# Optimization experiments

Hardware: AMD Instinct MI355X
Metric: run time of the kernel (lower is better)

The kernel has to match this reference:

```python
import jax, jax.numpy as jnp
import numpy as np

N, DM, F, G, FG = 4096, 512, 128, 8, 16
DH, DE, ES = 128, 256, 4
E = G * ES
GROUP_TOP_K, EXPERT_TOP_K = 2, 2
TEMP = 1.0
LN_EPS = 1e-5


def _ln(x, g, b):
    m = jnp.mean(x, axis=-1, keepdims=True)
    v = jnp.mean((x - m) ** 2, axis=-1, keepdims=True)
    return (x - m) * jax.lax.rsqrt(v + LN_EPS) * g + b


def _topk_softmax(logits, k):
    # faithful to torch _topk_softmax: softmax over top-k values, zeros elsewhere
    vals, idx = jax.lax.top_k(logits, k)
    w = jax.nn.softmax(vals, axis=-1)
    oh = jax.nn.one_hot(idx, logits.shape[-1], dtype=logits.dtype)  # [..., k, E]
    return jnp.einsum('...ke,...k->...e', oh, w)


def setup_inputs() -> dict:
    key = jax.random.key(0)
    ks = iter(jax.random.split(key, 32))
    n = lambda shape, s=0.02: jax.random.normal(next(ks), shape, dtype=jnp.float32) * s
    d = {
        'hidden': jax.random.normal(next(ks), (N, DM), dtype=jnp.float32),
        'feat': jax.random.normal(next(ks), (N, F), dtype=jnp.float32),
        # pre_ln
        'pre_ln_g': jnp.ones((DM,), jnp.float32), 'pre_ln_b': jnp.zeros((DM,), jnp.float32),
        # router_hidden_encoder: LN(DM) -> Lin(DM,DH) -> GELU -> Lin(DH,DH)
        'rh_ln_g': jnp.ones((DM,), jnp.float32), 'rh_ln_b': jnp.zeros((DM,), jnp.float32),
        'rh_w1': n((DM, DH)), 'rh_b1': jnp.zeros((DH,), jnp.float32),
        'rh_w2': n((DH, DH)), 'rh_b2': jnp.zeros((DH,), jnp.float32),
        # stage_feature_encoder: LN(F) -> Lin(F,DH) -> GELU -> Lin(DH,DH)
        'sf_ln_g': jnp.ones((F,), jnp.float32), 'sf_ln_b': jnp.zeros((F,), jnp.float32),
        'sf_w1': n((F, DH)), 'sf_b1': jnp.zeros((DH,), jnp.float32),
        'sf_w2': n((DH, DH)), 'sf_b2': jnp.zeros((DH,), jnp.float32),
        # group_feature_encoders (stacked over G): LN(FG) -> Lin(FG,DH) -> GELU -> Lin(DH,DH)
        'gf_ln_g': jnp.ones((G, FG), jnp.float32), 'gf_ln_b': jnp.zeros((G, FG), jnp.float32),
        'gf_w1': n((G, FG, DH)), 'gf_b1': jnp.zeros((G, DH), jnp.float32),
        'gf_w2': n((G, DH, DH)), 'gf_b2': jnp.zeros((G, DH), jnp.float32),
        # per_group_scorer (ScalarRouter): Lin(4DH,DH) -> GELU -> Lin(DH,1)
        'pgs_w1': n((4 * DH, DH)), 'pgs_b1': jnp.zeros((DH,), jnp.float32),
        'pgs_w2': n((DH,)), 'pgs_b2': jnp.zeros((), jnp.float32),
        # intra_routers (stacked over G): Lin(4DH,DH) -> GELU -> Lin(DH,ES)
        'ir_w1': n((G, 4 * DH, DH)), 'ir_b1': jnp.zeros((G, DH), jnp.float32),
        'ir_w2': n((G, DH, ES)), 'ir_b2': jnp.zeros((G, ES), jnp.float32),
        # experts (stacked over E = G*ES, group-major): Lin(DM,DE) -> GELU -> Lin(DE,DM)
        'ex_w1': n((E, DM, DE)), 'ex_b1': jnp.zeros((E, DE), jnp.float32),
        'ex_w2': n((E, DE, DM)), 'ex_b2': jnp.zeros((E, DM), jnp.float32),
    }
    return d


def reference(hidden, feat, pre_ln_g, pre_ln_b, rh_ln_g, rh_ln_b, rh_w1, rh_b1, rh_w2, rh_b2,
              sf_ln_g, sf_ln_b, sf_w1, sf_b1, sf_w2, sf_b2,
              gf_ln_g, gf_ln_b, gf_w1, gf_b1, gf_w2, gf_b2,
              pgs_w1, pgs_b1, pgs_w2, pgs_b2,
              ir_w1, ir_b1, ir_w2, ir_b2,
              ex_w1, ex_b1, ex_w2, ex_b2):
    # expert input (pre-LN hidden)
    h_norm = _ln(hidden, pre_ln_g, pre_ln_b)                         # [N, DM]

    # factorized router encoders
    h_enc = jax.nn.gelu(_ln(hidden, rh_ln_g, rh_ln_b) @ rh_w1 + rh_b1) @ rh_w2 + rh_b2   # [N, DH]
    s_enc = jax.nn.gelu(_ln(feat, sf_ln_g, sf_ln_b) @ sf_w1 + sf_b1) @ sf_w2 + sf_b2     # [N, DH]
    gfeat = feat.reshape(N, G, FG)                                    # disjoint contiguous group features
    g_h = jax.nn.gelu(jnp.einsum('ngf,gfh->ngh', _ln(gfeat, gf_ln_g, gf_ln_b), gf_w1) + gf_b1)
    g_enc = jnp.einsum('ngh,ghk->ngk', g_h, gf_w2) + gf_b2            # [N, G, DH]

    hB = jnp.broadcast_to(h_enc[:, None, :], (N, G, DH))
    sB = jnp.broadcast_to(s_enc[:, None, :], (N, G, DH))
    router_in = jnp.concatenate([hB, sB, g_enc, hB * g_enc], axis=-1)  # [N, G, 4DH]

    # per-group scalar scores -> group logits -> top-k scatter softmax
    pg_h = jax.nn.gelu(jnp.einsum('ngi,ih->ngh', router_in, pgs_w1) + pgs_b1)
    group_logits = (jnp.einsum('ngh,h->ng', pg_h, pgs_w2) + pgs_b2) / max(TEMP, 1e-6)    # [N, G]
    group_w = _topk_softmax(group_logits, GROUP_TOP_K)                 # [N, G]

    # intra-group expert routers -> top-k scatter softmax over expert_scale
    ir_h = jax.nn.gelu(jnp.einsum('ngi,gih->ngh', router_in, ir_w1) + ir_b1)
    intra_logits = jnp.einsum('ngh,ghe->nge', ir_h, ir_w2) + ir_b2     # [N, G, ES]
    intra_w = _topk_softmax(intra_logits, EXPERT_TOP_K)                # [N, G, ES]

    comb_w = (group_w[:, :, None] * intra_w).reshape(N, E)             # group-major expert order

    # per-expert GELU MLPs on pre-LN hidden (dense compute, sparse weights)
    eh = jax.nn.gelu(jnp.einsum('nd,edh->neh', h_norm, ex_w1) + ex_b1) # [N, E, DE]
    eo = jnp.einsum('neh,ehd->ned', eh, ex_w2) + ex_b2                 # [N, E, DM]
    out = jnp.einsum('ne,ned->nd', comb_w, eo)                         # [N, DM]
    return out
```

## Files before the change

kernel.cpp:

```cpp
#include <hip/hip_runtime.h>
#include <hip/hip_bf16.h>
#include <math.h>

#define N_TOK 4096
#define DM 512
#define FDIM 128
#define G 8
#define FG 16
#define DH 128
#define DE 256
#define ES 4
#define E_EXP 32
#define LN_EPS 1e-5f
#define BT 32

typedef __attribute__((ext_vector_type(8))) short bf16x8;
typedef __attribute__((ext_vector_type(4))) float f32x4;

#define MFMA16(a, b, c) __builtin_amdgcn_mfma_f32_16x16x32_bf16((a), (b), (c), 0, 0, 0)

__device__ __forceinline__ float gelu_t(float x) {
    const float c = 0.7978845608028654f;
    float x3 = x * x * x;
    return 0.5f * x * (1.0f + tanhf(c * (x + 0.044715f * x3)));
}

__device__ __forceinline__ short f2bf(float f) {
    __hip_bfloat16 h = __float2bfloat16(f);
    return *reinterpret_cast<short*>(&h);
}
__device__ __forceinline__ float bf2f(short s) {
    __hip_bfloat16 h = *reinterpret_cast<__hip_bfloat16*>(&s);
    return __bfloat162float(h);
}
__device__ __forceinline__ void split3(float x, short& h, short& m, short& l) {
    h = f2bf(x);
    float r = x - bf2f(h);
    m = f2bf(r);
    float r2 = r - bf2f(m);
    l = f2bf(r2);
}

struct ConvJob { const float* src; short* dh; short* dm; short* dl;
                 int KB, NB, Kreal, plain, blk0; };
struct ConvJobs { ConvJob j[10]; };

__global__ void k_pre(ConvJobs J, int nconv,
                      const float* __restrict__ hidden,
                      const float* __restrict__ pg, const float* __restrict__ pb,
                      const float* __restrict__ rg, const float* __restrict__ rb,
                      __hip_bfloat16* __restrict__ h_normb, float* __restrict__ hL) {
    int b = blockIdx.x;
    if (b >= nconv) {
        int n = b - nconv;
        int j = threadIdx.x;
        const float* x = hidden + (size_t)n * DM;
        float v0 = x[j], v1 = x[j + 256];
        float s = v0 + v1, q = v0 * v0 + v1 * v1;
#pragma unroll
        for (int o = 32; o; o >>= 1) { s += __shfl_down(s, o); q += __shfl_down(q, o); }
        __shared__ float red[8];
        int w = j >> 6;
        if ((j & 63) == 0) { red[w] = s; red[4 + w] = q; }
        __syncthreads();
        float sum = red[0] + red[1] + red[2] + red[3];
        float sq  = red[4] + red[5] + red[6] + red[7];
        float m = sum * (1.0f / DM);
        float var = sq * (1.0f / DM) - m * m;
        float rs = rsqrtf(var + LN_EPS);
        float t0 = (v0 - m) * rs, t1 = (v1 - m) * rs;
        size_t base = (size_t)n * DM;
        h_normb[base + j]       = __float2bfloat16(t0 * pg[j]       + pb[j]);
        h_normb[base + j + 256] = __float2bfloat16(t1 * pg[j + 256] + pb[j + 256]);
        hL[base + j]           = t0 * rg[j]       + rb[j];
        hL[base + j + 256]     = t1 * rg[j + 256] + rb[j + 256];
        return;
    }
    int ji = 0;
#pragma unroll
    for (int i = 1; i < 10; i++) if (b >= J.j[i].blk0) ji = i;
    const ConvJob jb = J.j[ji];
    int rel = b - jb.blk0;
    int mat = rel / jb.KB, kb = rel % jb.KB;
    int ncols = jb.NB * 16;
    const float* s = jb.src + (size_t)mat * jb.Kreal * ncols;
    size_t dbase = ((size_t)mat * jb.KB + kb) * jb.NB * 512;
    for (int p = threadIdx.x; p < jb.NB * 64; p += 256) {
        int nb = p >> 6, lane = p & 63;
        int row0 = kb * 32 + ((lane >> 4) << 3);
        int col = nb * 16 + (lane & 15);
        if (jb.plain) {
            union { short sh[8]; uint4 v; } t;
#pragma unroll
            for (int j = 0; j < 8; j++) {
                float x = (row0 + j < jb.Kreal) ? s[(size_t)(row0 + j) * ncols + col] : 0.f;
                t.sh[j] = f2bf(x);
            }
            *(uint4*)&jb.dh[dbase + (size_t)p * 8] = t.v;
        } else {
            union { short sh[8]; uint4 v; } hi, mi, lo;
#pragma unroll
            for (int j = 0; j < 8; j++) {
                float x = (row0 + j < jb.Kreal) ? s[(size_t)(row0 + j) * ncols + col] : 0.f;
                split3(x, hi.sh[j], mi.sh[j], lo.sh[j]);
            }
            *(uint4*)&jb.dh[dbase + (size_t)p * 8] = hi.v;
            *(uint4*)&jb.dm[dbase + (size_t)p * 8] = mi.v;
            *(uint4*)&jb.dl[dbase + (size_t)p * 8] = lo.v;
        }
    }
}

template <int KB_TOT, bool DO_LN>
__device__ __forceinline__ void enc2_body(
        int bx, char* smem,
        const float* __restrict__ X,
        const float* __restrict__ lng, const float* __restrict__ lnb,
        const short* __restrict__ W1h, const short* __restrict__ W1m, const short* __restrict__ W1l,
        const float* __restrict__ B1,
        const short* __restrict__ W2h, const short* __restrict__ W2m, const short* __restrict__ W2l,
        const float* __restrict__ B2,
        float* __restrict__ Y) {
    constexpr int K = KB_TOT * 32;
    const int n0 = bx * 32;
    const int tid = threadIdx.x;
    const int wave = tid >> 6, lane = tid & 63;
    const int quad = lane >> 4, lm = lane & 15;
    const int mt = wave & 1;
    const int ngb = (wave >> 1) * 4;

    short (*Ah)[132] = (short(*)[132])smem;
    short (*Am)[132] = (short(*)[132])(smem + 32 * 132 * 2);
    short (*Al)[132] = (short(*)[132])(smem + 2 * 32 * 132 * 2);

    f32x4 acc[4];
#pragma unroll
    for (int i = 0; i < 4; i++) acc[i] = (f32x4)(0.f);

    if (DO_LN) {
        for (int idx = tid; idx < 1024; idx += 256) {
            int row = idx >> 5, c4 = (idx & 31) * 4;
            float4 v = *(const float4*)&X[(size_t)(n0 + row) * K + c4];
            float s = v.x + v.y + v.z + v.w;
            float q = v.x * v.x + v.y * v.y + v.z * v.z + v.w * v.w;
#pragma unroll
            for (int o = 16; o; o >>= 1) { s += __shfl_xor(s, o); q += __shfl_xor(q, o); }
            float mean = s * (1.0f / 128.0f);
            float var = q * (1.0f / 128.0f) - mean * mean;
            float rs = rsqrtf(var + LN_EPS);
            float xv[4] = {(v.x - mean) * rs * lng[c4 + 0] + lnb[c4 + 0],
                           (v.y - mean) * rs * lng[c4 + 1] + lnb[c4 + 1],
                           (v.z - mean) * rs * lng[c4 + 2] + lnb[c4 + 2],
                           (v.w - mean) * rs * lng[c4 + 3] + lnb[c4 + 3]};
#pragma unroll
            for (int j = 0; j < 4; j++) {
                short h, m, l; split3(xv[j], h, m, l);
                Ah[row][c4 + j] = h; Am[row][c4 + j] = m; Al[row][c4 + j] = l;
            }
        }
        __syncthreads();
#pragma unroll
        for (int kb = 0; kb < KB_TOT; kb++) {
            bf16x8 ah = *(const bf16x8*)&Ah[mt * 16 + lm][kb * 32 + quad * 8];
            bf16x8 am = *(const bf16x8*)&Am[mt * 16 + lm][kb * 32 + quad * 8];
            bf16x8 al = *(const bf16x8*)&Al[mt * 16 + lm][kb * 32 + quad * 8];
#pragma unroll
            for (int nt = 0; nt < 4; nt++) {
                size_t bi = (((size_t)kb * 8 + ngb + nt) * 64 + lane) * 8;
                bf16x8 bh = *(const bf16x8*)&W1h[bi];
                bf16x8 bm = *(const bf16x8*)&W1m[bi];
                bf16x8 bl = *(const bf16x8*)&W1l[bi];
                acc[nt] = MFMA16(al, bh, acc[nt]);
                acc[nt] = MFMA16(am, bm, acc[nt]);
                acc[nt] = MFMA16(ah, bl, acc[nt]);
                acc[nt] = MFMA16(am, bh, acc[nt]);
                acc[nt] = MFMA16(ah, bm, acc[nt]);
                acc[nt] = MFMA16(ah, bh, acc[nt]);
            }
        }
    } else {
        for (int kb = 0; kb < KB_TOT; kb++) {
            const float* xs = X + (size_t)(n0 + mt * 16 + lm) * K + kb * 32 + quad * 8;
            float4 x0 = *(const float4*)xs, x1 = *(const float4*)(xs + 4);
            float xv[8] = {x0.x, x0.y, x0.z, x0.w, x1.x, x1.y, x1.z, x1.w};
            bf16x8 ah, am, al;
#pragma unroll
            for (int j = 0; j < 8; j++) {
                short h, m, l; split3(xv[j], h, m, l);
                ah[j] = h; am[j] = m; al[j] = l;
            }
#pragma unroll
            for (int nt = 0; nt < 4; nt++) {
                size_t bi = (((size_t)kb * 8 + ngb + nt) * 64 + lane) * 8;
                bf16x8 bh = *(const bf16x8*)&W1h[bi];
                bf16x8 bm = *(const bf16x8*)&W1m[bi];
                bf16x8 bl = *(const bf16x8*)&W1l[bi];
                acc[nt] = MFMA16(al, bh, acc[nt]);
                acc[nt] = MFMA16(am, bm, acc[nt]);
                acc[nt] = MFMA16(ah, bl, acc[nt]);
                acc[nt] = MFMA16(am, bh, acc[nt]);
                acc[nt] = MFMA16(ah, bm, acc[nt]);
                acc[nt] = MFMA16(ah, bh, acc[nt]);
            }
        }
    }
    __syncthreads();
#pragma unroll
    for (int nt = 0; nt < 4; nt++) {
        int col = (ngb + nt) * 16 + lm;
        float b1 = B1[col];
#pragma unroll
        for (int r = 0; r < 4; r++) {
            int row = mt * 16 + quad * 4 + r;
            short h, m, l; split3(gelu_t(acc[nt][r] + b1), h, m, l);
            Ah[row][col] = h; Am[row][col] = m; Al[row][col] = l;
        }
    }
    __syncthreads();
    f32x4 acc2[4];
#pragma unroll
    for (int i = 0; i < 4; i++) acc2[i] = (f32x4)(0.f);
#pragma unroll
    for (int kb = 0; kb < 4; kb++) {
        bf16x8 ah = *(const bf16x8*)&Ah[mt * 16 + lm][kb * 32 + quad * 8];
        bf16x8 am = *(const bf16x8*)&Am[mt * 16 + lm][kb * 32 + quad * 8];
        bf16x8 al = *(const bf16x8*)&Al[mt * 16 + lm][kb * 32 + quad * 8];
#pragma unroll
        for (int nt = 0; nt < 4; nt++) {
            size_t bi = (((size_t)kb * 8 + ngb + nt) * 64 + lane) * 8;
            bf16x8 bh = *(const bf16x8*)&W2h[bi];
            bf16x8 bm = *(const bf16x8*)&W2m[bi];
            bf16x8 bl = *(const bf16x8*)&W2l[bi];
            acc2[nt] = MFMA16(al, bh, acc2[nt]);
            acc2[nt] = MFMA16(am, bm, acc2[nt]);
            acc2[nt] = MFMA16(ah, bl, acc2[nt]);
            acc2[nt] = MFMA16(am, bh, acc2[nt]);
            acc2[nt] = MFMA16(ah, bm, acc2[nt]);
            acc2[nt] = MFMA16(ah, bh, acc2[nt]);
        }
    }
#pragma unroll
    for (int nt = 0; nt < 4; nt++) {
        int col = (ngb + nt) * 16 + lm;
        float b2 = B2[col];
#pragma unroll
        for (int r = 0; r < 4; r++) {
            int row = mt * 16 + quad * 4 + r;
            Y[(size_t)(n0 + row) * DH + col] = acc2[nt][r] + b2;
        }
    }
}

__device__ __forceinline__ void genc_one(
        int bx, int g, char* smem,
        const float* __restrict__ feat,
        const float* __restrict__ gln_g, const float* __restrict__ gln_b,
        const short* __restrict__ W1h, const short* __restrict__ W1m, const short* __restrict__ W1l,
        const float* __restrict__ gb1,
        const short* __restrict__ W2h, const short* __restrict__ W2m, const short* __restrict__ W2l,
        const float* __restrict__ gb2,
        float* __restrict__ g_enc) {
    const int tid = threadIdx.x;
    const int wave = tid >> 6, lane = tid & 63;
    const int quad = lane >> 4, lm = lane & 15;
    const int mt = wave & 1;
    const int ngb = (wave >> 1) * 4;
    const int n0 = bx * 32;

    short (*Ah)[132] = (short(*)[132])smem;
    short (*Am)[132] = (short(*)[132])(smem + 8448);
    short (*Al)[132] = (short(*)[132])(smem + 2 * 8448);

    {
        int t = tid >> 3, sub = tid & 7;
        const float* fr = feat + (size_t)(n0 + t) * FDIM + g * FG;
        float xv[FG];
        float mean = 0.f;
#pragma unroll
        for (int i = 0; i < FG; i++) { xv[i] = fr[i]; mean += xv[i]; }
        mean *= (1.0f / FG);
        float var = 0.f;
#pragma unroll
        for (int i = 0; i < FG; i++) { float d = xv[i] - mean; var += d * d; }
        var *= (1.0f / FG);
        float rs = rsqrtf(var + LN_EPS);
#pragma unroll
        for (int j = 0; j < 2; j++) {
            int i = sub * 2 + j;
            float xn = (xv[i] - mean) * rs * gln_g[g * FG + i] + gln_b[g * FG + i];
            short h, m, l; split3(xn, h, m, l);
            Ah[t][i] = h; Am[t][i] = m; Al[t][i] = l;
            Ah[t][16 + i] = 0; Am[t][16 + i] = 0; Al[t][16 + i] = 0;
        }
    }
    __syncthreads();
    f32x4 acc[4];
#pragma unroll
    for (int i = 0; i < 4; i++) acc[i] = (f32x4)(0.f);
    {
        bf16x8 ah = *(const bf16x8*)&Ah[mt * 16 + lm][quad * 8];
        bf16x8 am = *(const bf16x8*)&Am[mt * 16 + lm][quad * 8];
        bf16x8 al = *(const bf16x8*)&Al[mt * 16 + lm][quad * 8];
#pragma unroll
        for (int nt = 0; nt < 4; nt++) {
            size_t bi = (((size_t)g * 8 + ngb + nt) * 64 + lane) * 8;
            bf16x8 bh = *(const bf16x8*)&W1h[bi];
            bf16x8 bm = *(const bf16x8*)&W1m[bi];
            bf16x8 bl = *(const bf16x8*)&W1l[bi];
            acc[nt] = MFMA16(al, bh, acc[nt]);
            acc[nt] = MFMA16(am, bm, acc[nt]);
            acc[nt] = MFMA16(ah, bl, acc[nt]);
            acc[nt] = MFMA16(am, bh, acc[nt]);
            acc[nt] = MFMA16(ah, bm, acc[nt]);
            acc[nt] = MFMA16(ah, bh, acc[nt]);
        }
    }
    __syncthreads();
#pragma unroll
    for (int nt = 0; nt < 4; nt++) {
        int col = (ngb + nt) * 16 + lm;
        float b1 = gb1[g * DH + col];
#pragma unroll
        for (int r = 0; r < 4; r++) {
            int row = mt * 16 + quad * 4 + r;
            short h, m, l; split3(gelu_t(acc[nt][r] + b1), h, m, l);
            Ah[row][col] = h; Am[row][col] = m; Al[row][col] = l;
        }
    }
    __syncthreads();
    f32x4 acc2[4];
#pragma unroll
    for (int i = 0; i < 4; i++) acc2[i] = (f32x4)(0.f);
#pragma unroll
    for (int kb = 0; kb < 4; kb++) {
        bf16x8 a2h = *(const bf16x8*)&Ah[mt * 16 + lm][kb * 32 + quad * 8];
        bf16x8 a2m = *(const bf16x8*)&Am[mt * 16 + lm][kb * 32 + quad * 8];
        bf16x8 a2l = *(const bf16x8*)&Al[mt * 16 + lm][kb * 32 + quad * 8];
#pragma unroll
        for (int nt = 0; nt < 4; nt++) {
            size_t bi = ((((size_t)g * 4 + kb) * 8 + ngb + nt) * 64 + lane) * 8;
            bf16x8 bh = *(const bf16x8*)&W2h[bi];
            bf16x8 bm = *(const bf16x8*)&W2m[bi];
            bf16x8 bl = *(const bf16x8*)&W2l[bi];
            acc2[nt] = MFMA16(a2l, bh, acc2[nt]);
            acc2[nt] = MFMA16(a2m, bm, acc2[nt]);
            acc2[nt] = MFMA16(a2h, bl, acc2[nt]);
            acc2[nt] = MFMA16(a2m, bh, acc2[nt]);
            acc2[nt] = MFMA16(a2h, bm, acc2[nt]);
            acc2[nt] = MFMA16(a2h, bh, acc2[nt]);
        }
    }
#pragma unroll
    for (int nt = 0; nt < 4; nt++) {
        int col = (ngb + nt) * 16 + lm;
        float b2 = gb2[g * DH + col];
#pragma unroll
        for (int r = 0; r < 4; r++) {
            int row = mt * 16 + quad * 4 + r;
            g_enc[((size_t)(n0 + row) * G + g) * DH + col] = acc2[nt][r] + b2;
        }
    }
}

__global__ __launch_bounds__(256) void k_enc_all(
        const float* __restrict__ hL, const float* __restrict__ feat,
        const float* __restrict__ sf_g, const float* __restrict__ sf_b,
        const float* __restrict__ gln_g, const float* __restrict__ gln_b,
        const short* Brh1H, const short* Brh1M, const short* Brh1L, const float* rh_b1,
        const short* Brh2H, const short* Brh2M, const short* Brh2L, const float* rh_b2,
        const short* Bsf1H, const short* Bsf1M, const short* Bsf1L, const float* sf_b1,
        const short* Bsf2H, const short* Bsf2M, const short* Bsf2L, const float* sf_b2,
        const short* Bgf1H, const short* Bgf1M, const short* Bgf1L, const float* gf_b1,
        const short* Bgf2H, const short* Bgf2M, const short* Bgf2L, const float* gf_b2,
        float* __restrict__ h_enc, float* __restrict__ s_enc, float* __restrict__ g_enc) {
    __shared__ __align__(16) char smem[3 * 8448];
    int bid = blockIdx.x;
    if (bid < 128)
        enc2_body<16, false>(bid, smem, hL, nullptr, nullptr,
                             Brh1H, Brh1M, Brh1L, rh_b1, Brh2H, Brh2M, Brh2L, rh_b2, h_enc);
    else if (bid < 256)
        enc2_body<4, true>(bid - 128, smem, feat, sf_g, sf_b,
                           Bsf1H, Bsf1M, Bsf1L, sf_b1, Bsf2H, Bsf2M, Bsf2L, sf_b2, s_enc);
    else {
        int idx = bid - 256;
        genc_one(idx >> 3, idx & 7, smem, feat, gln_g, gln_b,
                 Bgf1H, Bgf1M, Bgf1L, gf_b1, Bgf2H, Bgf2M, Bgf2L, gf_b2, g_enc);
    }
}

__device__ __forceinline__ void stage16v(float4 a, float4 b, float4 c, float4 d,
                                         char* smem, int wo0, int wo1) {
    float v0[8] = {a.x, a.y, a.z, a.w, b.x, b.y, b.z, b.w};
    float v1[8] = {c.x, c.y, c.z, c.w, d.x, d.y, d.z, d.w};
    bf16x8 h0, m0, l0, h1, m1, l1;
#pragma unroll
    for (int j = 0; j < 8; j++) { short hh, mm, ll; split3(v0[j], hh, mm, ll); h0[j]=hh; m0[j]=mm; l0[j]=ll; }
#pragma unroll
    for (int j = 0; j < 8; j++) { short hh, mm, ll; split3(v1[j], hh, mm, ll); h1[j]=hh; m1[j]=mm; l1[j]=ll; }
    *(bf16x8*)(smem + wo0) = h0;           *(bf16x8*)(smem + wo1) = h1;
    *(bf16x8*)(smem + 16384 + wo0) = m0;   *(bf16x8*)(smem + 16384 + wo1) = m1;
    *(bf16x8*)(smem + 32768 + wo0) = l0;   *(bf16x8*)(smem + 32768 + wo1) = l1;
}

__global__ __launch_bounds__(512) void k_router_mfma(
        const float* __restrict__ h_enc, const float* __restrict__ s_enc,
        const float* __restrict__ g_enc,
        const short* __restrict__ BpgH, const short* __restrict__ BpgM, const short* __restrict__ BpgL,
        const short* __restrict__ BirH, const short* __restrict__ BirM, const short* __restrict__ BirL,
        const float* __restrict__ pb1, const float* __restrict__ pw2, const float* __restrict__ pb2,
        const float* __restrict__ ib1, const float* __restrict__ iw2, const float* __restrict__ ib2,
        float* __restrict__ glog, float* __restrict__ ilog) {
    const int g = blockIdx.x & 7;
    const int bx = blockIdx.x >> 3;
    const int n0 = bx * 64;
    const int tid = threadIdx.x;
    const int wave = tid >> 6, lane = tid & 63;
    const int quad = lane >> 4, lm = lane & 15;
    const bool is_pg = wave < 4;
    const int nbase = (wave & 3) * 2;
    const short* Bh = is_pg ? BpgH : (BirH + (size_t)g * 65536);
    const short* Bm = is_pg ? BpgM : (BirM + (size_t)g * 65536);
    const short* Bl = is_pg ? BpgL : (BirL + (size_t)g * 65536);

    __shared__ __align__(16) char smem[49152];

    const int sr = tid >> 3, scb = tid & 7;
    const float* hrow = h_enc + (size_t)(n0 + sr) * DH + scb * 16;
    const float* srow = s_enc + (size_t)(n0 + sr) * DH + scb * 16;
    const float* grow = g_enc + ((size_t)(n0 + sr) * G + g) * DH + scb * 16;
    const int skbl = scb >> 1, st16 = sr >> 4, slm = sr & 15, sq0 = (scb & 1) * 2;
    const int wo0 = skbl * 4096 + st16 * 1024 + (sq0 * 16 + slm) * 16;
    const int wo1 = wo0 + 256;

    f32x4 acc[4][2];
#pragma unroll
    for (int mt = 0; mt < 4; mt++)
#pragma unroll
        for (int nt = 0; nt < 2; nt++) acc[mt][nt] = (f32x4)(0.f);

    float4 A0, A1, A2, A3;

#define LOAD4(P) { const float4* p4_ = (const float4*)(P); \
                   A0 = p4_[0]; A1 = p4_[1]; A2 = p4_[2]; A3 = p4_[3]; }
#define COMPUTE_CHUNK(CH) { _Pragma("unroll") \
    for (int kbl = 0; kbl < 4; kbl++) { \
        const int kb = (CH) * 4 + kbl; \
        bf16x8 Ahf[4], Amf[4], Alf[4]; \
        _Pragma("unroll") \
        for (int mt = 0; mt < 4; mt++) { \
            size_t loff = (size_t)kbl * 4096 + mt * 1024 + (size_t)lane * 16; \
            Ahf[mt] = *(const bf16x8*)(smem + loff); \
            Amf[mt] = *(const bf16x8*)(smem + 16384 + loff); \
            Alf[mt] = *(const bf16x8*)(smem + 32768 + loff); \
        } \
        _Pragma("unroll") \
        for (int nt = 0; nt < 2; nt++) { \
            size_t bi = (((size_t)kb * 8 + nbase + nt) * 64 + lane) * 8; \
            bf16x8 bh = *(const bf16x8*)&Bh[bi]; \
            bf16x8 bm = *(const bf16x8*)&Bm[bi]; \
            bf16x8 bl = *(const bf16x8*)&Bl[bi]; \
            _Pragma("unroll") \
            for (int mt = 0; mt < 4; mt++) { \
                acc[mt][nt] = MFMA16(Alf[mt], bh, acc[mt][nt]); \
                acc[mt][nt] = MFMA16(Amf[mt], bm, acc[mt][nt]); \
                acc[mt][nt] = MFMA16(Ahf[mt], bl, acc[mt][nt]); \
                acc[mt][nt] = MFMA16(Amf[mt], bh, acc[mt][nt]); \
                acc[mt][nt] = MFMA16(Ahf[mt], bm, acc[mt][nt]); \
                acc[mt][nt] = MFMA16(Ahf[mt], bh, acc[mt][nt]); \
            } \
        } \
    } }

    LOAD4(hrow);
    stage16v(A0, A1, A2, A3, smem, wo0, wo1);
    __syncthreads();
    LOAD4(srow);
    COMPUTE_CHUNK(0);

    __syncthreads();
    stage16v(A0, A1, A2, A3, smem, wo0, wo1);
    __syncthreads();
    LOAD4(grow);
    COMPUTE_CHUNK(1);

    __syncthreads();
    stage16v(A0, A1, A2, A3, smem, wo0, wo1);
    __syncthreads();
    float4 H0, H1, H2, H3;
    { const float4* p4_ = (const float4*)hrow; H0 = p4_[0]; H1 = p4_[1]; H2 = p4_[2]; H3 = p4_[3]; }
    COMPUTE_CHUNK(2);

    __syncthreads();
    {
        bf16x8 gh0 = *(const bf16x8*)(smem + wo0),          gh1 = *(const bf16x8*)(smem + wo1);
        bf16x8 gm0 = *(const bf16x8*)(smem + 16384 + wo0),  gm1 = *(const bf16x8*)(smem + 16384 + wo1);
        bf16x8 gl0 = *(const bf16x8*)(smem + 32768 + wo0),  gl1 = *(const bf16x8*)(smem + 32768 + wo1);
        float gv[16];
#pragma unroll
        for (int j = 0; j < 8; j++) gv[j]     = bf2f(gh0[j]) + bf2f(gm0[j]) + bf2f(gl0[j]);
#pragma unroll
        for (int j = 0; j < 8; j++) gv[8 + j] = bf2f(gh1[j]) + bf2f(gm1[j]) + bf2f(gl1[j]);
        float4 P0 = make_float4(H0.x * gv[0],  H0.y * gv[1],  H0.z * gv[2],  H0.w * gv[3]);
        float4 P1 = make_float4(H1.x * gv[4],  H1.y * gv[5],  H1.z * gv[6],  H1.w * gv[7]);
        float4 P2 = make_float4(H2.x * gv[8],  H2.y * gv[9],  H2.z * gv[10], H2.w * gv[11]);
        float4 P3 = make_float4(H3.x * gv[12], H3.y * gv[13], H3.z * gv[14], H3.w * gv[15]);
        stage16v(P0, P1, P2, P3, smem, wo0, wo1);
    }
    __syncthreads();
    COMPUTE_CHUNK(3);

#undef LOAD4
#undef COMPUTE_CHUNK

    float (*ph)[129] = (float(*)[129])smem;
    float (*ih)[129] = (float(*)[129])(smem + 32 * 129 * 4);
    for (int h = 0; h < 2; h++) {
        __syncthreads();
#pragma unroll
        for (int mi = 0; mi < 2; mi++) {
            int mt = 2 * h + mi;
#pragma unroll
            for (int nt = 0; nt < 2; nt++) {
                int col = (nbase + nt) * 16 + lm;
                float b1 = is_pg ? pb1[col] : ib1[g * DH + col];
                float* dst = is_pg ? &ph[0][0] : &ih[0][0];
#pragma unroll
                for (int r = 0; r < 4; r++) {
                    int row = mi * 16 + quad * 4 + r;
                    dst[row * 129 + col] = gelu_t(acc[mt][nt][r] + b1);
                }
            }
        }
        __syncthreads();
        if (tid < 128) {
            int t = tid >> 2, q = tid & 3;
            float s = 0.f;
            for (int i = q * 32; i < q * 32 + 32; i++) s += ph[t][i] * pw2[i];
            s += __shfl_xor(s, 1);
            s += __shfl_xor(s, 2);
            if (q == 0) glog[(size_t)(n0 + h * 32 + t) * G + g] = s + pb2[0];
        } else if (tid < 384) {
            int t2 = tid - 128;
            int t = t2 >> 3, e = (t2 >> 1) & 3, half = t2 & 1;
            const float* wv = iw2 + (size_t)g * DH * ES;
            float s = 0.f;
            for (int i = half * 64; i < half * 64 + 64; i++) s += ih[t][i] * wv[i * ES + e];
            s += __shfl_xor(s, 1);
            if (half == 0) ilog[((size_t)(n0 + h * 32 + t) * G + g) * ES + e] = s + ib2[g * ES + e];
        }
    }
}

__global__ void k_topk(const float* __restrict__ glog, const float* __restrict__ ilog,
                       int* __restrict__ cnt, int* __restrict__ toks, float* __restrict__ wgts) {
    int n = blockIdx.x * blockDim.x + threadIdx.x;
    if (n >= N_TOK) return;
    float gl[G];
#pragma unroll
    for (int g = 0; g < G; g++) gl[g] = glog[(size_t)n * G + g];
    int i1 = 0; float v1 = gl[0];
#pragma unroll
    for (int g = 1; g < G; g++) if (gl[g] > v1) { v1 = gl[g]; i1 = g; }
    int i2 = -1; float v2 = -1e30f;
#pragma unroll
    for (int g = 0; g < G; g++) if (g != i1 && gl[g] > v2) { v2 = gl[g]; i2 = g; }
    float eg = expf(v2 - v1);
    float den = 1.0f / (1.0f + eg);
    float gw_sel[2] = { den, eg * den };
    int g_sel[2] = { i1, i2 };
#pragma unroll
    for (int s = 0; s < 2; s++) {
        int g = g_sel[s]; float gw = gw_sel[s];
        float il[ES];
#pragma unroll
        for (int e = 0; e < ES; e++) il[e] = ilog[((size_t)n * G + g) * ES + e];
        int j1 = 0; float u1 = il[0];
#pragma unroll
        for (int e = 1; e < ES; e++) if (il[e] > u1) { u1 = il[e]; j1 = e; }
        int j2 = -1; float u2 = -1e30f;
#pragma unroll
        for (int e = 0; e < ES; e++) if (e != j1 && il[e] > u2) { u2 = il[e]; j2 = e; }
        float ei = expf(u2 - u1);
        float d2 = 1.0f / (1.0f + ei);
        int ex1 = g * ES + j1, ex2 = g * ES + j2;
        int p1 = atomicAdd(&cnt[ex1], 1);
        toks[(size_t)ex1 * N_TOK + p1] = n * 4 + s * 2;     wgts[(size_t)ex1 * N_TOK + p1] = gw * d2;
        int p2 = atomicAdd(&cnt[ex2], 1);
        toks[(size_t)ex2 * N_TOK + p2] = n * 4 + s * 2 + 1; wgts[(size_t)ex2 * N_TOK + p2] = gw * ei * d2;
    }
}

__global__ __launch_bounds__(512) void k_expert_mfma(
        const __hip_bfloat16* __restrict__ h_normb,
        const short* __restrict__ wB1, const float* __restrict__ eb1,
        const short* __restrict__ wB2, const float* __restrict__ eb2,
        const int* __restrict__ cnt, const int* __restrict__ toks,
        const float* __restrict__ wgts, float* __restrict__ part) {
    const int e = blockIdx.x & 31;
    const int slot = blockIdx.x >> 5;
    const int c = cnt[e];
    const int start = slot * BT;
    if (start >= c) return;
    const int m = min(BT, c - start);

    __shared__ short hs[BT][520];
    short (*es)[264] = (short(*)[264])&hs[0][0];
    __shared__ int   tok_s[BT];
    __shared__ float w_s[BT];

    const int tid = threadIdx.x;
    if (tid < BT) {
        bool ok = tid < m;
        tok_s[tid] = ok ? toks[(size_t)e * N_TOK + start + tid] : 0;
        w_s[tid]   = ok ? wgts[(size_t)e * N_TOK + start + tid] : 0.f;
    }
    __syncthreads();
    for (int idx = tid; idx < BT * 64; idx += 512) {
        int t = idx >> 6, ch = idx & 63;
        uint4 v = make_uint4(0, 0, 0, 0);
        if (t < m) v = *((const uint4*)(h_normb + (size_t)(tok_s[t] >> 2) * DM) + ch);
        *(uint4*)&hs[t][ch * 8] = v;
    }
    __syncthreads();

    const int wave = tid >> 6, lane = tid & 63;
    const int quad = lane >> 4, lm = lane & 15;

    const int ng = wave * 2;
    f32x4 acc1[2][2];
#pragma unroll
    for (int a = 0; a < 2; a++)
#pragma unroll
        for (int b = 0; b < 2; b++) acc1[a][b] = (f32x4)(0.f);
    {
        const short* w1e = wB1 + (size_t)e * DM * DE;
        for (int kb = 0; kb < 16; kb++) {
            bf16x8 a0 = *(const bf16x8*)&hs[lm][kb * 32 + quad * 8];
            bf16x8 a1 = *(const bf16x8*)&hs[16 + lm][kb * 32 + quad * 8];
            const short* wp = w1e + ((size_t)kb * 16 + ng) * 512 + lane * 8;
#pragma unroll
            for (int nt = 0; nt < 2; nt++) {
                bf16x8 b = *(const bf16x8*)(wp + nt * 512);
                acc1[0][nt] = MFMA16(a0, b, acc1[0][nt]);
                acc1[1][nt] = MFMA16(a1, b, acc1[1][nt]);
            }
        }
    }
    __syncthreads();
#pragma unroll
    for (int nt = 0; nt < 2; nt++) {
        int col = (ng + nt) * 16 + lm;
        float b1 = eb1[e * DE + col];
#pragma unroll
        for (int mt = 0; mt < 2; mt++)
#pragma unroll
        for (int r = 0; r < 4; r++) {
            int row = mt * 16 + quad * 4 + r;
            es[row][col] = f2bf(gelu_t(acc1[mt][nt][r] + b1));
        }
    }
    __syncthreads();

    {
        const int ng2 = wave * 4;
        f32x4 acc[2][4];
#pragma unroll
        for (int a = 0; a < 2; a++)
#pragma unroll
            for (int b = 0; b < 4; b++) acc[a][b] = (f32x4)(0.f);
        const short* w2e = wB2 + (size_t)e * DE * DM;
        for (int kb = 0; kb < 8; kb++) {
            bf16x8 a0 = *(const bf16x8*)&es[lm][kb * 32 + quad * 8];
            bf16x8 a1 = *(const bf16x8*)&es[16 + lm][kb * 32 + quad * 8];
            const short* wp = w2e + ((size_t)kb * 32 + ng2) * 512 + lane * 8;
#pragma unroll
            for (int nt = 0; nt < 4; nt++) {
                bf16x8 b = *(const bf16x8*)(wp + nt * 512);
                acc[0][nt] = MFMA16(a0, b, acc[0][nt]);
                acc[1][nt] = MFMA16(a1, b, acc[1][nt]);
            }
        }
        const float* b2 = eb2 + (size_t)e * DM;
#pragma unroll
        for (int mt = 0; mt < 2; mt++)
#pragma unroll
        for (int r = 0; r < 4; r++) {
            int row = mt * 16 + quad * 4 + r;
            if (row < m) {
                float w = w_s[row];
                float* prow = part + (size_t)tok_s[row] * DM;
#pragma unroll
                for (int nt = 0; nt < 4; nt++) {
                    int col = (ng2 + nt) * 16 + lm;
                    prow[col] = w * (acc[mt][nt][r] + b2[col]);
                }
            }
        }
    }
}

__global__ void k_reduce(const float* __restrict__ part, float* __restrict__ out) {
    int n = blockIdx.x;
    int j = threadIdx.x;
    const float4* p = (const float4*)(part + (size_t)n * 4 * DM);
    float4 a = p[j], b = p[128 + j], c = p[256 + j], d = p[384 + j];
    float4 r = make_float4(a.x + b.x + c.x + d.x, a.y + b.y + c.y + d.y,
                           a.z + b.z + c.z + d.z, a.w + b.w + c.w + d.w);
    ((float4*)(out + (size_t)n * DM))[j] = r;
}

extern "C" void kernel_launch(void* const* d_in, const int* in_sizes, int n_in,
                              void* d_out, int out_size, void* d_ws, size_t ws_size,
                              hipStream_t stream) {
    const float* hidden  = (const float*)d_in[0];
    const float* feat    = (const float*)d_in[1];
    const float* pre_g   = (const float*)d_in[2];
    const float* pre_b   = (const float*)d_in[3];
    const float* rh_g    = (const float*)d_in[4];
    const float* rh_b    = (const float*)d_in[5];
    const float* rh_w1   = (const float*)d_in[6];
    const float* rh_b1   = (const float*)d_in[7];
    const float* rh_w2   = (const float*)d_in[8];
    const float* rh_b2   = (const float*)d_in[9];
    const float* sf_g    = (const float*)d_in[10];
    const float* sf_b    = (const float*)d_in[11];
    const float* sf_w1   = (const float*)d_in[12];
    const float* sf_b1   = (const float*)d_in[13];
    const float* sf_w2   = (const float*)d_in[14];
    const float* sf_b2   = (const float*)d_in[15];
    const float* gln_g   = (const float*)d_in[16];
    const float* gln_b   = (const float*)d_in[17];
    const float* gf_w1   = (const float*)d_in[18];
    const float* gf_b1   = (const float*)d_in[19];
    const float* gf_w2   = (const float*)d_in[20];
    const float* gf_b2   = (const float*)d_in[21];
    const float* pgs_w1  = (const float*)d_in[22];
    const float* pgs_b1  = (const float*)d_in[23];
    const float* pgs_w2  = (const float*)d_in[24];
    const float* pgs_b2  = (const float*)d_in[25];
    const float* ir_w1   = (const float*)d_in[26];
    const float* ir_b1   = (const float*)d_in[27];
    const float* ir_w2   = (const float*)d_in[28];
    const float* ir_b2   = (const float*)d_in[29];
    const float* ex_w1   = (const float*)d_in[30];
    const float* ex_b1   = (const float*)d_in[31];
    const float* ex_w2   = (const float*)d_in[32];
    const float* ex_b2   = (const float*)d_in[33];
    float* out = (float*)d_out;

    char* w = (char*)d_ws;
    auto alloc = [&](size_t bytes) { void* r = (void*)w; w += (bytes + 255) & ~(size_t)255; return r; };
    __hip_bfloat16* h_normb = (__hip_bfloat16*)alloc((size_t)N_TOK * DM * 2);
    float* h_enc = (float*)alloc((size_t)N_TOK * DH * 4);
    float* s_enc = (float*)alloc((size_t)N_TOK * DH * 4);
    float* g_enc = (float*)alloc((size_t)N_TOK * G * DH * 4);
    float* glog  = (float*)alloc((size_t)N_TOK * G * 4);
    float* ilog  = (float*)alloc((size_t)N_TOK * G * ES * 4);
    float* wgts  = (float*)alloc((size_t)E_EXP * N_TOK * 4);
    short* wB1   = (short*)alloc((size_t)E_EXP * DM * DE * 2);
    short* wB2   = (short*)alloc((size_t)E_EXP * DE * DM * 2);
    short* BpgH  = (short*)alloc((size_t)16 * 8 * 512 * 2);
    short* BpgM  = (short*)alloc((size_t)16 * 8 * 512 * 2);
    short* BpgL  = (short*)alloc((size_t)16 * 8 * 512 * 2);
    short* BirH  = (short*)alloc((size_t)G * 16 * 8 * 512 * 2);
    short* BirM  = (short*)alloc((size_t)G * 16 * 8 * 512 * 2);
    short* BirL  = (short*)alloc((size_t)G * 16 * 8 * 512 * 2);
    short* Brh1H = (short*)alloc((size_t)16 * 8 * 512 * 2);
    short* Brh1M = (short*)alloc((size_t)16 * 8 * 512 * 2);
    short* Brh1L = (short*)alloc((size_t)16 * 8 * 512 * 2);
    short* Brh2H = (short*)alloc((size_t)4 * 8 * 512 * 2);
    short* Brh2M = (short*)alloc((size_t)4 * 8 * 512 * 2);
    short* Brh2L = (short*)alloc((size_t)4 * 8 * 512 * 2);
    short* Bsf1H = (short*)alloc((size_t)4 * 8 * 512 * 2);
    short* Bsf1M = (short*)alloc((size_t)4 * 8 * 512 * 2);
    short* Bsf1L = (short*)alloc((size_t)4 * 8 * 512 * 2);
    short* Bsf2H = (short*)alloc((size_t)4 * 8 * 512 * 2);
    short* Bsf2M = (short*)alloc((size_t)4 * 8 * 512 * 2);
    short* Bsf2L = (short*)alloc((size_t)4 * 8 * 512 * 2);
    short* Bgf1H = (short*)alloc((size_t)G * 1 * 8 * 512 * 2);
    short* Bgf1M = (short*)alloc((size_t)G * 1 * 8 * 512 * 2);
    short* Bgf1L = (short*)alloc((size_t)G * 1 * 8 * 512 * 2);
    short* Bgf2H = (short*)alloc((size_t)G * 4 * 8 * 512 * 2);
    short* Bgf2M = (short*)alloc((size_t)G * 4 * 8 * 512 * 2);
    short* Bgf2L = (short*)alloc((size_t)G * 4 * 8 * 512 * 2);
    int* cnt     = (int*)alloc(E_EXP * 4);
    int* toks    = (int*)alloc((size_t)E_EXP * N_TOK * 4);
    char* uni   = (char*)alloc((size_t)N_TOK * 4 * DM * 4);
    float* hL   = (float*)uni;
    float* part = (float*)uni;

    hipMemsetAsync(cnt, 0, E_EXP * sizeof(int), stream);

    ConvJobs J;
    int b0 = 0;
    auto mkjob = [&](int i, const float* s, short* dh, short* dm, short* dl,
                     int KB, int NB, int Kreal, int plain, int nmat) {
        J.j[i] = ConvJob{s, dh, dm, dl, KB, NB, Kreal, plain, b0};
        b0 += KB * nmat;
    };
    mkjob(0, ex_w1, wB1, nullptr, nullptr, 16, 16, 512, 1, E_EXP);
    mkjob(1, ex_w2, wB2, nullptr, nullptr, 8, 32, 256, 1, E_EXP);
    mkjob(2, pgs_w1, BpgH, BpgM, BpgL, 16, 8, 512, 0, 1);
    mkjob(3, ir_w1, BirH, BirM, BirL, 16, 8, 512, 0, G);
    mkjob(4, rh_w1, Brh1H, Brh1M, Brh1L, 16, 8, 512, 0, 1);
    mkjob(5, rh_w2, Brh2H, Brh2M, Brh2L, 4, 8, 128, 0, 1);
    mkjob(6, sf_w1, Bsf1H, Bsf1M, Bsf1L, 4, 8, 128, 0, 1);
    mkjob(7, sf_w2, Bsf2H, Bsf2M, Bsf2L, 4, 8, 128, 0, 1);
    mkjob(8, gf_w1, Bgf1H, Bgf1M, Bgf1L, 1, 8, 16, 0, G);
    mkjob(9, gf_w2, Bgf2H, Bgf2M, Bgf2L, 4, 8, 128, 0, G);
    k_pre<<<b0 + N_TOK, 256, 0, stream>>>(J, b0, hidden, pre_g, pre_b, rh_g, rh_b, h_normb, hL);

    k_enc_all<<<256 + (N_TOK / 32) * G, 256, 0, stream>>>(
        hL, feat, sf_g, sf_b, gln_g, gln_b,
        Brh1H, Brh1M, Brh1L, rh_b1, Brh2H, Brh2M, Brh2L, rh_b2,
        Bsf1H, Bsf1M, Bsf1L, sf_b1, Bsf2H, Bsf2M, Bsf2L, sf_b2,
        Bgf1H, Bgf1M, Bgf1L, gf_b1, Bgf2H, Bgf2M, Bgf2L, gf_b2,
        h_enc, s_enc, g_enc);

    k_router_mfma<<<(N_TOK / 64) * G, 512, 0, stream>>>(h_enc, s_enc, g_enc,
                                             BpgH, BpgM, BpgL, BirH, BirM, BirL,
                                             pgs_b1, pgs_w2, pgs_b2, ir_b1, ir_w2, ir_b2,
                                             glog, ilog);

    k_topk<<<N_TOK / 256, 256, 0, stream>>>(glog, ilog, cnt, toks, wgts);
    k_expert_mfma<<<(N_TOK / BT) * E_EXP, 512, 0, stream>>>(h_normb, wB1, ex_b1, wB2, ex_b2,
                                                            cnt, toks, wgts, part);
    k_reduce<<<N_TOK, 128, 0, stream>>>(part, out);
}
```

Measured before the change: 336.2 us.

## Shrink router tile to 32 tokens, swizzle LDS, convert next chunk before barrier

The router kernel now uses 32-token tiles with 256 threads. Each wave computes 2x4 MFMA tiles instead of 4x2, and the LDS footprint is halved. Staging stores and fragment loads use an XOR swizzle to cut LDS bank conflicts. The bf16 split of the next chunk is done in registers before the barrier, so conversion overlaps better with compute. This doubles the grid and occupancy but halves the reuse of each B-fragment global load per token.

```diff
diff --git a/kernel.cpp b/kernel.cpp
--- a/kernel.cpp
+++ b/kernel.cpp
@@ -388,21 +388,7 @@
     }
 }
 
-__device__ __forceinline__ void stage16v(float4 a, float4 b, float4 c, float4 d,
-                                         char* smem, int wo0, int wo1) {
-    float v0[8] = {a.x, a.y, a.z, a.w, b.x, b.y, b.z, b.w};
-    float v1[8] = {c.x, c.y, c.z, c.w, d.x, d.y, d.z, d.w};
-    bf16x8 h0, m0, l0, h1, m1, l1;
-#pragma unroll
-    for (int j = 0; j < 8; j++) { short hh, mm, ll; split3(v0[j], hh, mm, ll); h0[j]=hh; m0[j]=mm; l0[j]=ll; }
-#pragma unroll
-    for (int j = 0; j < 8; j++) { short hh, mm, ll; split3(v1[j], hh, mm, ll); h1[j]=hh; m1[j]=mm; l1[j]=ll; }
-    *(bf16x8*)(smem + wo0) = h0;           *(bf16x8*)(smem + wo1) = h1;
-    *(bf16x8*)(smem + 16384 + wo0) = m0;   *(bf16x8*)(smem + 16384 + wo1) = m1;
-    *(bf16x8*)(smem + 32768 + wo0) = l0;   *(bf16x8*)(smem + 32768 + wo1) = l1;
-}
-
-__global__ __launch_bounds__(512) void k_router_mfma(
+__global__ __launch_bounds__(256) void k_router_mfma(
         const float* __restrict__ h_enc, const float* __restrict__ s_enc,
         const float* __restrict__ g_enc,
         const short* __restrict__ BpgH, const short* __restrict__ BpgM, const short* __restrict__ BpgL,
@@ -412,55 +398,70 @@
         float* __restrict__ glog, float* __restrict__ ilog) {
     const int g = blockIdx.x & 7;
     const int bx = blockIdx.x >> 3;
-    const int n0 = bx * 64;
+    const int n0 = bx * 32;
     const int tid = threadIdx.x;
     const int wave = tid >> 6, lane = tid & 63;
     const int quad = lane >> 4, lm = lane & 15;
-    const bool is_pg = wave < 4;
-    const int nbase = (wave & 3) * 2;
+    const bool is_pg = wave < 2;
+    const int nbase = (wave & 1) * 4;
     const short* Bh = is_pg ? BpgH : (BirH + (size_t)g * 65536);
     const short* Bm = is_pg ? BpgM : (BirM + (size_t)g * 65536);
     const short* Bl = is_pg ? BpgL : (BirL + (size_t)g * 65536);
 
-    __shared__ __align__(16) char smem[49152];
+    __shared__ __align__(16) char smem[24576];
 
     const int sr = tid >> 3, scb = tid & 7;
     const float* hrow = h_enc + (size_t)(n0 + sr) * DH + scb * 16;
     const float* srow = s_enc + (size_t)(n0 + sr) * DH + scb * 16;
     const float* grow = g_enc + ((size_t)(n0 + sr) * G + g) * DH + scb * 16;
     const int skbl = scb >> 1, st16 = sr >> 4, slm = sr & 15, sq0 = (scb & 1) * 2;
-    const int wo0 = skbl * 4096 + st16 * 1024 + (sq0 * 16 + slm) * 16;
-    const int wo1 = wo0 + 256;
-
-    f32x4 acc[4][2];
-#pragma unroll
-    for (int mt = 0; mt < 4; mt++)
-#pragma unroll
-        for (int nt = 0; nt < 2; nt++) acc[mt][nt] = (f32x4)(0.f);
+    const int woA = skbl * 2048 + st16 * 1024 + (sq0 * 16 + slm) * 16;
+    const int woB = woA + 256;
+#define SWZ(a) ((a) ^ ((((a) >> 11) & 3) << 5) ^ ((((a) >> 9) & 1) << 4))
+    const int swA = SWZ(woA), swB = SWZ(woB);
+    const int rx4 = ((lane >> 5) & 1) << 4;
+
+    f32x4 acc[2][4];
+#pragma unroll
+    for (int mt = 0; mt < 2; mt++)
+#pragma unroll
+        for (int nt = 0; nt < 4; nt++) acc[mt][nt] = (f32x4)(0.f);
 
     float4 A0, A1, A2, A3;
-
-#define LOAD4(P) { const float4* p4_ = (const float4*)(P); \
-                   A0 = p4_[0]; A1 = p4_[1]; A2 = p4_[2]; A3 = p4_[3]; }
+    bf16x8 F0, F1, F2, F3, F4, F5;
+
+#define LOAD4A(P) { const float4* p4_ = (const float4*)(P); \
+                    A0 = p4_[0]; A1 = p4_[1]; A2 = p4_[2]; A3 = p4_[3]; }
+#define CONVA() { \
+    float v0_[8] = {A0.x, A0.y, A0.z, A0.w, A1.x, A1.y, A1.z, A1.w}; \
+    float v1_[8] = {A2.x, A2.y, A2.z, A2.w, A3.x, A3.y, A3.z, A3.w}; \
+    _Pragma("unroll") \
+    for (int j = 0; j < 8; j++) { short hh, mm, ll; split3(v0_[j], hh, mm, ll); F0[j]=hh; F1[j]=mm; F2[j]=ll; } \
+    _Pragma("unroll") \
+    for (int j = 0; j < 8; j++) { short hh, mm, ll; split3(v1_[j], hh, mm, ll); F3[j]=hh; F4[j]=mm; F5[j]=ll; } }
+#define WRF() { \
+    *(bf16x8*)(smem + swA)         = F0; *(bf16x8*)(smem + swB)         = F3; \
+    *(bf16x8*)(smem +  8192 + swA) = F1; *(bf16x8*)(smem +  8192 + swB) = F4; \
+    *(bf16x8*)(smem + 16384 + swA) = F2; *(bf16x8*)(smem + 16384 + swB) = F5; }
 #define COMPUTE_CHUNK(CH) { _Pragma("unroll") \
     for (int kbl = 0; kbl < 4; kbl++) { \
         const int kb = (CH) * 4 + kbl; \
-        bf16x8 Ahf[4], Amf[4], Alf[4]; \
+        bf16x8 Ahf[2], Amf[2], Alf[2]; \
         _Pragma("unroll") \
-        for (int mt = 0; mt < 4; mt++) { \
-            size_t loff = (size_t)kbl * 4096 + mt * 1024 + (size_t)lane * 16; \
-            Ahf[mt] = *(const bf16x8*)(smem + loff); \
-            Amf[mt] = *(const bf16x8*)(smem + 16384 + loff); \
-            Alf[mt] = *(const bf16x8*)(smem + 32768 + loff); \
+        for (int mt = 0; mt < 2; mt++) { \
+            int lo = ((kbl * 2048 + mt * 1024 + lane * 16) ^ (kbl << 5)) ^ rx4; \
+            Ahf[mt] = *(const bf16x8*)(smem + lo); \
+            Amf[mt] = *(const bf16x8*)(smem + 8192 + lo); \
+            Alf[mt] = *(const bf16x8*)(smem + 16384 + lo); \
         } \
         _Pragma("unroll") \
-        for (int nt = 0; nt < 2; nt++) { \
+        for (int nt = 0; nt < 4; nt++) { \
             size_t bi = (((size_t)kb * 8 + nbase + nt) * 64 + lane) * 8; \
             bf16x8 bh = *(const bf16x8*)&Bh[bi]; \
             bf16x8 bm = *(const bf16x8*)&Bm[bi]; \
             bf16x8 bl = *(const bf16x8*)&Bl[bi]; \
             _Pragma("unroll") \
-            for (int mt = 0; mt < 4; mt++) { \
+            for (int mt = 0; mt < 2; mt++) { \
                 acc[mt][nt] = MFMA16(Alf[mt], bh, acc[mt][nt]); \
                 acc[mt][nt] = MFMA16(Amf[mt], bm, acc[mt][nt]); \
                 acc[mt][nt] = MFMA16(Ahf[mt], bl, acc[mt][nt]); \
@@ -471,82 +472,83 @@
         } \
     } }
 
-    LOAD4(hrow);
-    stage16v(A0, A1, A2, A3, smem, wo0, wo1);
-    __syncthreads();
-    LOAD4(srow);
+    LOAD4A(hrow); CONVA(); WRF();
+    __syncthreads();
+    LOAD4A(srow);
     COMPUTE_CHUNK(0);
-
-    __syncthreads();
-    stage16v(A0, A1, A2, A3, smem, wo0, wo1);
-    __syncthreads();
-    LOAD4(grow);
+    CONVA();
+    __syncthreads();
+    WRF();
+    __syncthreads();
+
+    LOAD4A(grow);
     COMPUTE_CHUNK(1);
-
-    __syncthreads();
-    stage16v(A0, A1, A2, A3, smem, wo0, wo1);
-    __syncthreads();
+    CONVA();
+    __syncthreads();
+    WRF();
+    __syncthreads();
+
     float4 H0, H1, H2, H3;
     { const float4* p4_ = (const float4*)hrow; H0 = p4_[0]; H1 = p4_[1]; H2 = p4_[2]; H3 = p4_[3]; }
     COMPUTE_CHUNK(2);
-
-    __syncthreads();
     {
-        bf16x8 gh0 = *(const bf16x8*)(smem + wo0),          gh1 = *(const bf16x8*)(smem + wo1);
-        bf16x8 gm0 = *(const bf16x8*)(smem + 16384 + wo0),  gm1 = *(const bf16x8*)(smem + 16384 + wo1);
-        bf16x8 gl0 = *(const bf16x8*)(smem + 32768 + wo0),  gl1 = *(const bf16x8*)(smem + 32768 + wo1);
-        float gv[16];
-#pragma unroll
-        for (int j = 0; j < 8; j++) gv[j]     = bf2f(gh0[j]) + bf2f(gm0[j]) + bf2f(gl0[j]);
-#pragma unroll
-        for (int j = 0; j < 8; j++) gv[8 + j] = bf2f(gh1[j]) + bf2f(gm1[j]) + bf2f(gl1[j]);
-        float4 P0 = make_float4(H0.x * gv[0],  H0.y * gv[1],  H0.z * gv[2],  H0.w * gv[3]);
-        float4 P1 = make_float4(H1.x * gv[4],  H1.y * gv[5],  H1.z * gv[6],  H1.w * gv[7]);
-        float4 P2 = make_float4(H2.x * gv[8],  H2.y * gv[9],  H2.z * gv[10], H2.w * gv[11]);
-        float4 P3 = make_float4(H3.x * gv[12], H3.y * gv[13], H3.z * gv[14], H3.w * gv[15]);
-        stage16v(P0, P1, P2, P3, smem, wo0, wo1);
-    }
-    __syncthreads();
+        bf16x8 gh0 = *(const bf16x8*)(smem + swA),         gh1 = *(const bf16x8*)(smem + swB);
+        bf16x8 gm0 = *(const bf16x8*)(smem + 8192 + swA),  gm1 = *(const bf16x8*)(smem + 8192 + swB);
+        bf16x8 gl0 = *(const bf16x8*)(smem + 16384 + swA), gl1 = *(const bf16x8*)(smem + 16384 + swB);
+        float gv0[8], gv1[8];
+#pragma unroll
+        for (int j = 0; j < 8; j++) gv0[j] = bf2f(gh0[j]) + bf2f(gm0[j]) + bf2f(gl0[j]);
+#pragma unroll
+        for (int j = 0; j < 8; j++) gv1[j] = bf2f(gh1[j]) + bf2f(gm1[j]) + bf2f(gl1[j]);
+        A0 = make_float4(H0.x * gv0[0], H0.y * gv0[1], H0.z * gv0[2], H0.w * gv0[3]);
+        A1 = make_float4(H1.x * gv0[4], H1.y * gv0[5], H1.z * gv0[6], H1.w * gv0[7]);
+        A2 = make_float4(H2.x * gv1[0], H2.y * gv1[1], H2.z * gv1[2], H2.w * gv1[3]);
+        A3 = make_float4(H3.x * gv1[4], H3.y * gv1[5], H3.z * gv1[6], H3.w * gv1[7]);
+        CONVA();
+    }
+    __syncthreads();
+    WRF();
+    __syncthreads();
+
     COMPUTE_CHUNK(3);
 
-#undef LOAD4
+#undef LOAD4A
+#undef CONVA
+#undef WRF
 #undef COMPUTE_CHUNK
+#undef SWZ
 
     float (*ph)[129] = (float(*)[129])smem;
-    float (*ih)[129] = (float(*)[129])(smem + 32 * 129 * 4);
+    float (*ih)[129] = (float(*)[129])(smem + 16 * 129 * 4);
     for (int h = 0; h < 2; h++) {
         __syncthreads();
 #pragma unroll
-        for (int mi = 0; mi < 2; mi++) {
-            int mt = 2 * h + mi;
-#pragma unroll
-            for (int nt = 0; nt < 2; nt++) {
-                int col = (nbase + nt) * 16 + lm;
-                float b1 = is_pg ? pb1[col] : ib1[g * DH + col];
-                float* dst = is_pg ? &ph[0][0] : &ih[0][0];
-#pragma unroll
-                for (int r = 0; r < 4; r++) {
-                    int row = mi * 16 + quad * 4 + r;
-                    dst[row * 129 + col] = gelu_t(acc[mt][nt][r] + b1);
-                }
+        for (int nt = 0; nt < 4; nt++) {
+            int col = (nbase + nt) * 16 + lm;
+            float b1 = is_pg ? pb1[col] : ib1[g * DH + col];
+            float* dst = is_pg ? &ph[0][0] : &ih[0][0];
+#pragma unroll
+            for (int r = 0; r < 4; r++) {
+                int row = quad * 4 + r;
+                dst[row * 129 + col] = gelu_t(acc[h][nt][r] + b1);
             }
         }
         __syncthreads();
-        if (tid < 128) {
+        if (tid < 64) {
             int t = tid >> 2, q = tid & 3;
             float s = 0.f;
             for (int i = q * 32; i < q * 32 + 32; i++) s += ph[t][i] * pw2[i];
             s += __shfl_xor(s, 1);
             s += __shfl_xor(s, 2);
-            if (q == 0) glog[(size_t)(n0 + h * 32 + t) * G + g] = s + pb2[0];
-        } else if (tid < 384) {
-            int t2 = tid - 128;
+            if (q == 0) glog[(size_t)(n0 + h * 16 + t) * G + g] = s + pb2[0];
+        } else if (tid < 192) {
+            int t2 = tid - 64;
             int t = t2 >> 3, e = (t2 >> 1) & 3, half = t2 & 1;
             const float* wv = iw2 + (size_t)g * DH * ES;
             float s = 0.f;
             for (int i = half * 64; i < half * 64 + 64; i++) s += ih[t][i] * wv[i * ES + e];
             s += __shfl_xor(s, 1);
-            if (half == 0) ilog[((size_t)(n0 + h * 32 + t) * G + g) * ES + e] = s + ib2[g * ES + e];
+            if (half == 0) ilog[((size_t)(n0 + h * 16 + t) * G + g) * ES + e] = s + ib2[g * ES + e];
         }
     }
 }
@@ -817,7 +819,7 @@
         Bgf1H, Bgf1M, Bgf1L, gf_b1, Bgf2H, Bgf2M, Bgf2L, gf_b2,
         h_enc, s_enc, g_enc);
 
-    k_router_mfma<<<(N_TOK / 64) * G, 512, 0, stream>>>(h_enc, s_enc, g_enc,
+    k_router_mfma<<<(N_TOK / 32) * G, 256, 0, stream>>>(h_enc, s_enc, g_enc,
                                              BpgH, BpgM, BpgL, BirH, BirM, BirL,
                                              pgs_b1, pgs_w2, pgs_b2, ir_b1, ir_w2, ir_b2,
                                              glog, ilog);
```

Result: slower. 367.9 us (+9.4%).
